# Kernel optimization log

Measured on AMD Instinct MI355X. Metric: run time of the kernel, lower is better.

## Reference

```python
import jax, jax.numpy as jnp
import numpy as np

B, T, C = 4, 2048, 1024
H = 16
D = C // H          # 64 head dim
CS = 128            # chunk_size (hard-coded in module)


def setup_inputs() -> dict:
    key = jax.random.key(0)
    ks = jax.random.split(key, 6)
    scale = 0.02
    x = jax.random.normal(ks[0], (B, T, C), dtype=jnp.float32)
    Wq = jax.random.normal(ks[1], (C, C), dtype=jnp.float32) * scale
    Wk = jax.random.normal(ks[2], (C, C), dtype=jnp.float32) * scale
    Wv = jax.random.normal(ks[3], (C, C), dtype=jnp.float32) * scale
    Wo = jax.random.normal(ks[4], (C, C), dtype=jnp.float32) * scale
    alpha_raw = jnp.zeros((1, H, 1, 1), dtype=jnp.float32)
    beta_raw = jnp.zeros((1, H, 1, 1), dtype=jnp.float32)
    return {"x": x, "Wq": Wq, "Wk": Wk, "Wv": Wv, "Wo": Wo,
            "alpha_raw": alpha_raw, "beta_raw": beta_raw}


def reference(x, Wq, Wk, Wv, Wo, alpha_raw, beta_raw):
    Bb, Tt, Cc = x.shape
    nc = Tt // CS
    N = Bb * H * nc  # flattened (batch, head, chunk) recurrence lanes

    # projections -> [B, H, T, D]
    def proj(W):
        return (x @ W).reshape(Bb, Tt, H, D).transpose(0, 2, 1, 3)
    q, k, v = proj(Wq), proj(Wk), proj(Wv)
    # F.normalize(k, dim=-1) with eps=1e-12
    k = k / jnp.maximum(jnp.linalg.norm(k, axis=-1, keepdims=True), 1e-12)

    alpha = jax.nn.sigmoid(alpha_raw).reshape(H) * 0.5  # [H]
    beta = jax.nn.sigmoid(beta_raw).reshape(H) * 0.5    # [H]
    a = jnp.broadcast_to(alpha[None, :, None], (Bb, H, nc)).reshape(N, 1, 1)
    b = jnp.broadcast_to(beta[None, :, None], (Bb, H, nc)).reshape(N, 1, 1)

    # chunk layout [CS, N, D] for time-major scan
    def to_scan(u):
        return u.reshape(Bb, H, nc, CS, D).reshape(N, CS, D).transpose(1, 0, 2)
    qc, kc, vc = to_scan(q), to_scan(k), to_scan(v)

    # --- per-chunk operators: A = prod(I - a k k^T), B accumulates writes ---
    def op_step(carry, kv):
        A, Bo = carry
        kt, vt = kv  # [N, D]
        Ak = jnp.einsum('nij,nj->ni', A, kt)
        A = A - a * (Ak[:, :, None] * kt[:, None, :])
        Bk = jnp.einsum('nij,nj->ni', Bo, kt)
        Bo = Bo - a * (Bk[:, :, None] * kt[:, None, :]) + b * (vt[:, :, None] * kt[:, None, :])
        return (A, Bo), None

    A0 = jnp.broadcast_to(jnp.eye(D, dtype=x.dtype), (N, D, D))
    (Aop, Bop), _ = jax.lax.scan(op_step, (A0, jnp.zeros((N, D, D), x.dtype)), (kc, vc))

    # --- inter-chunk scan: M_{i+1} = M_i A_i + B_i ---
    Aop_c = Aop.reshape(Bb, H, nc, D, D).transpose(2, 0, 1, 3, 4)
    Bop_c = Bop.reshape(Bb, H, nc, D, D).transpose(2, 0, 1, 3, 4)

    def chunk_step(M, ab):
        Ai, Bi = ab
        return jnp.einsum('bhij,bhjk->bhik', M, Ai) + Bi, M

    M_final, M_starts = jax.lax.scan(
        chunk_step, jnp.zeros((Bb, H, D, D), x.dtype), (Aop_c, Bop_c))

    # --- intra-chunk application: y_t = M_t q_t; rank-1 delta update ---
    M0 = M_starts.transpose(1, 2, 0, 3, 4).reshape(N, D, D)

    def proc_step(M, qkv):
        qt, kt, vt = qkv
        yt = jnp.einsum('nij,nj->ni', M, qt)  # == q_t @ M^T (inference path)
        Mk = jnp.einsum('nij,nj->ni', M, kt)
        M = M - a * (Mk[:, :, None] * kt[:, None, :]) + b * (vt[:, :, None] * kt[:, None, :])
        return M, yt

    _, ys = jax.lax.scan(proc_step, M0, (qc, kc, vc))  # [CS, N, D]
    y = ys.transpose(1, 0, 2).reshape(Bb, H, Tt, D)
    y = y.transpose(0, 2, 1, 3).reshape(Bb, Tt, Cc)
    y = y @ Wo  # c_proj (dropout=0 -> identity)
    return (y, M_final)
```

## Files before the change

### kernel.cpp

```cpp
#include <hip/hip_runtime.h>
#include <stdint.h>


#define DEV __device__ __forceinline__

typedef __attribute__((ext_vector_type(4))) float f32x4;
typedef __attribute__((ext_vector_type(8))) __bf16 bf16x8;
typedef __attribute__((ext_vector_type(4))) __bf16 bf16x4;

typedef const __attribute__((address_space(1))) uint32_t* gas1_t;
typedef __attribute__((address_space(3))) uint32_t* las3_t;

DEV void gload_lds16(const void* g, void* l) {
  __builtin_amdgcn_global_load_lds((gas1_t)g, (las3_t)l, 16, 0, 0);
}

DEV float sgm(float x) { return 1.f / (1.f + __expf(-x)); }

template <int CTRL>
DEV float dpp_mov(float x) {
  return __builtin_bit_cast(
      float, __builtin_amdgcn_mov_dpp(__builtin_bit_cast(int, x), CTRL, 0xF, 0xF, true));
}
DEV float row16_reduce(float x) {
  x += dpp_mov<0x121>(x);
  x += dpp_mov<0x122>(x);
  x += dpp_mov<0x124>(x);
  x += dpp_mov<0x128>(x);
  return x;
}

DEV int swzb(int row, int col, int stride) {
  return ((row * stride + col) << 1) ^ ((row & 7) << 4);
}
DEV bf16x8 ldfrag(const __bf16* B, int row, int col, int stride) {
  return *(const bf16x8*)((const char*)B + swzb(row, col, stride));
}
DEV __bf16 ldsc(const __bf16* B, int row, int col, int stride) {
  return *(const __bf16*)((const char*)B + swzb(row, col, stride));
}
DEV void stb(__bf16* B, int row, int col, int stride, __bf16 v) {
  *(__bf16*)((char*)B + swzb(row, col, stride)) = v;
}
DEV void stb4(__bf16* B, int row, int c4, int stride, bf16x4 v) {
  *(bf16x4*)((char*)B + swzb(row, c4, stride)) = v;
}
DEV int goffn(int tr) {
  int m = tr >> 1;
  return (tr & 1) ? (2 * m * m + 4 * m + 2) : (2 * m * m + 2 * m);
}
DEV int stile(int tr, int sc) { return ((tr * (tr + 1)) / 2 + sc) * 256; }

__global__ __launch_bounds__(256) void cast_f32_bf16(const float* __restrict__ in,
                                                     __bf16* __restrict__ out) {
  int idx = blockIdx.x * 256 + threadIdx.x;
  float4 v = ((const float4*)in)[idx];
  bf16x4 o;
  o[0] = (__bf16)v.x; o[1] = (__bf16)v.y; o[2] = (__bf16)v.z; o[3] = (__bf16)v.w;
  ((bf16x4*)out)[idx] = o;
}

__global__ __launch_bounds__(256) void transpose_cast4(const float* __restrict__ W0,
                                                       const float* __restrict__ W1,
                                                       const float* __restrict__ W2,
                                                       const float* __restrict__ W3,
                                                       __bf16* __restrict__ Wt) {
  const float* W = (blockIdx.z == 0) ? W0 : (blockIdx.z == 1) ? W1
                   : (blockIdx.z == 2) ? W2 : W3;
  __bf16* dst = Wt + ((size_t)blockIdx.z << 20);
  __shared__ float tile[32][33];
  int tx = threadIdx.x & 31, ty = threadIdx.x >> 5;
  int n0 = blockIdx.x * 32, k0 = blockIdx.y * 32;
#pragma unroll
  for (int u = 0; u < 4; ++u)
    tile[ty + u * 8][tx] = W[(size_t)(k0 + ty + u * 8) * 1024 + n0 + tx];
  __syncthreads();
#pragma unroll
  for (int u = 0; u < 4; ++u)
    dst[(size_t)(n0 + ty + u * 8) * 1024 + k0 + tx] = (__bf16)tile[tx][ty + u * 8];
}

DEV int ghash(int row) { return (row ^ (row >> 2)) & 3; }
DEV void stage_tile32(const __bf16* __restrict__ G, __bf16* L, int t, int wid, int K) {
#pragma unroll
  for (int it = 0; it < 2; ++it) {
    int e = it * 256 + t;
    int row = e >> 2;
    int c0 = ((e & 3) ^ ghash(row)) << 3;
    gload_lds16(G + (size_t)row * K + c0, L + it * 2048 + wid * 512);
  }
}
DEV bf16x8 ldfrag32(const __bf16* L, int row, int fkq) {
  return *(const bf16x8*)(L + row * 32 + ((fkq ^ ghash(row)) << 3));
}

__global__ __launch_bounds__(256, 3) void gemm_bt(const __bf16* __restrict__ A,
                                                  const __bf16* __restrict__ Bt,
                                                  float* __restrict__ Cf,
                                                  __bf16* __restrict__ Cb,
                                                  int mode, int NBN) {
  const int t = threadIdx.x;
  const int wid = t >> 6, lane = t & 63;
  const int fr = lane & 15, fkq = lane >> 4;
  const int wr = wid >> 1, wc = wid & 1;
  const int K = 1024;
  int nwg = gridDim.x, lin = blockIdx.x;
  int q = nwg >> 3;
  int id2 = (lin & 7) * q + (lin >> 3);
  int bn = id2 % NBN, bm = id2 / NBN;
  __shared__ __bf16 lA[3][4096];
  __shared__ __bf16 lB[3][4096];
  const __bf16* Ab = A + (size_t)(bm * 128) * K;
  const __bf16* Bb = Bt + (size_t)(bn * 128) * K;
  f32x4 acc[4][4];
#pragma unroll
  for (int m = 0; m < 4; ++m)
#pragma unroll
    for (int nn = 0; nn < 4; ++nn) acc[m][nn] = 0.f;
  stage_tile32(Ab, lA[0], t, wid, K);
  stage_tile32(Bb, lB[0], t, wid, K);
  stage_tile32(Ab + 32, lA[1], t, wid, K);
  stage_tile32(Bb + 32, lB[1], t, wid, K);
  int cur = 0;
  for (int kt = 0; kt < 32; ++kt) {
    asm volatile("s_barrier" ::: "memory");
    if (kt + 2 < 32) {
      int nxt = cur >= 1 ? cur - 1 : cur + 2;
      stage_tile32(Ab + (kt + 2) * 32, lA[nxt], t, wid, K);
      stage_tile32(Bb + (kt + 2) * 32, lB[nxt], t, wid, K);
      asm volatile("s_waitcnt vmcnt(8)" ::: "memory");
    } else if (kt + 1 < 32) {
      asm volatile("s_waitcnt vmcnt(4)" ::: "memory");
    } else {
      asm volatile("s_waitcnt vmcnt(0)" ::: "memory");
    }
    asm volatile("s_barrier" ::: "memory");
    bf16x8 af[4], bg[4];
#pragma unroll
    for (int m = 0; m < 4; ++m)
      af[m] = ldfrag32(lA[cur], wr * 64 + m * 16 + fr, fkq);
#pragma unroll
    for (int nn = 0; nn < 4; ++nn)
      bg[nn] = ldfrag32(lB[cur], wc * 64 + nn * 16 + fr, fkq);
#pragma unroll
    for (int m = 0; m < 4; ++m)
#pragma unroll
      for (int nn = 0; nn < 4; ++nn)
        acc[m][nn] =
            __builtin_amdgcn_mfma_f32_16x16x32_bf16(af[m], bg[nn], acc[m][nn], 0, 0, 0);
    cur = (cur < 2) ? cur + 1 : 0;
  }
#pragma unroll
  for (int m = 0; m < 4; ++m) {
#pragma unroll
    for (int nn = 0; nn < 4; ++nn) {
#pragma unroll
      for (int rg = 0; rg < 4; ++rg) {
        int row = bm * 128 + wr * 64 + m * 16 + fkq * 4 + rg;
        int col = bn * 128 + wc * 64 + nn * 16 + fr;
        float val = acc[m][nn][rg];
        if (mode == 0) {
          Cf[(size_t)row * 1024 + col] = val;
        } else {
          int buf = col >> 10, cc = col & 1023;
          int b = row >> 11, tk = row & 2047;
          int h = cc >> 6, d = cc & 63;
          Cb[(size_t)buf * 8388608 + (((size_t)b * 16 + h) * 2048 + tk) * 64 + d] =
              (__bf16)val;
        }
      }
    }
  }
}

__global__ __launch_bounds__(512, 6) void wy_ab(const __bf16* __restrict__ kb,
                                                const __bf16* __restrict__ vb,
                                                const float* __restrict__ ar,
                                                const float* __restrict__ br,
                                                __bf16* __restrict__ Ug,
                                                __bf16* __restrict__ Wgb,
                                                __bf16* __restrict__ ATg,
                                                __bf16* __restrict__ Bop) {
  int n = blockIdx.x, h = (n >> 4) & 15;
  float a = sgm(ar[h]) * 0.5f;
  float b = sgm(br[h]) * 0.5f;
  int t = threadIdx.x, wid = t >> 6, lane = t & 63;
  int fr = lane & 15, fkq = lane >> 4, fk = fkq * 8;
  __shared__ __attribute__((aligned(16))) char pool[51200];
  __bf16* Ks  = (__bf16*)pool;
  __bf16* MTu = (__bf16*)pool;
  __bf16* MTw = (__bf16*)(pool + 16384);
  __bf16* Sng = (__bf16*)(pool + 32768);
  __bf16* KT  = (__bf16*)(pool + 32768);
  const __bf16* kg = kb + (size_t)n * 8192;
  const __bf16* vg = vb + (size_t)n * 8192;
  bf16x8 zz;
#pragma unroll
  for (int e = 0; e < 8; ++e) zz[e] = (__bf16)0.f;
  f32x4 c0 = {0.f, 0.f, 0.f, 0.f};
  bf16x4 kreg[4];
#pragma unroll
  for (int it = 0; it < 4; ++it) {
    int u = it * 512 + t;
    int row = u >> 4, c4 = (u & 15) * 4;
    bf16x4 kh = ((const bf16x4*)kg)[u];
    float kf[4];
#pragma unroll
    for (int e = 0; e < 4; ++e) kf[e] = (float)kh[e];
    float ssq = kf[0] * kf[0] + kf[1] * kf[1] + kf[2] * kf[2] + kf[3] * kf[3];
    ssq = row16_reduce(ssq);
    float inv = 1.f / fmaxf(sqrtf(ssq), 1e-12f);
    bf16x4 kn;
#pragma unroll
    for (int e = 0; e < 4; ++e) kn[e] = (__bf16)(kf[e] * inv);
    kreg[it] = kn;
    stb4(Ks, row, c4, 64, kn);
  }
  __syncthreads();
  for (int p = wid; p < 36; p += 8) {
    int tr = 0, pp = p;
    while (pp > tr) { pp -= (tr + 1); ++tr; }
    int sc = pp;
    f32x4 acc = {0.f, 0.f, 0.f, 0.f};
#pragma unroll
    for (int ks = 0; ks < 2; ++ks)
      acc = __builtin_amdgcn_mfma_f32_16x16x32_bf16(
          ldfrag(Ks, tr * 16 + fr, ks * 32 + fk, 64),
          ldfrag(Ks, sc * 16 + fr, ks * 32 + fk, 64), acc, 0, 0, 0);
    __bf16* dst = Sng + stile(tr, sc);
#pragma unroll
    for (int rg = 0; rg < 4; ++rg) {
      int r = fkq * 4 + rg;
      float v = -a * acc[rg];
      if (tr == sc && fr >= r) v = 0.f;
      dst[r * 16 + fr] = (__bf16)v;
    }
  }
  f32x4 U[4], W[4];
#pragma unroll
  for (int ct = 0; ct < 4; ++ct) {
#pragma unroll
    for (int rg = 0; rg < 4; ++rg) {
      int row = wid * 16 + fkq * 4 + rg, col = ct * 16 + fr;
      U[ct][rg] = (float)ldsc(Ks, row, col, 64);
      W[ct][rg] = b * (float)vg[row * 64 + col];
    }
  }
  __syncthreads();
  {
    __bf16* scr  = ((__bf16*)pool) + wid * 2048;
    __bf16* tNT  = scr;
    __bf16* tN2R = scr + 256;
    __bf16* tN2T = scr + 512;
    __bf16* tN4R = scr + 768;
    __bf16* tN4T = scr + 1024;
    __bf16* tN8T = scr + 1280;
    __bf16* tPR  = scr + 1536;
    __bf16* Nd = Sng + stile(wid, wid);
    float nv[4];
#pragma unroll
    for (int rg = 0; rg < 4; ++rg) {
      nv[rg] = (float)Nd[(fkq * 4 + rg) * 16 + fr];
      tNT[fr * 16 + fkq * 4 + rg] = (__bf16)nv[rg];
    }
    asm volatile("s_waitcnt lgkmcnt(0)" ::: "memory");
    bf16x8 af = (fk < 16) ? *(const bf16x8*)(Nd + fr * 16 + fk) : zz;
    bf16x8 bop = (fk < 16) ? *(const bf16x8*)(tNT + fr * 16 + fk) : zz;
    f32x4 X = __builtin_amdgcn_mfma_f32_16x16x32_bf16(af, bop, c0, 0, 0, 0);
#pragma unroll
    for (int rg = 0; rg < 4; ++rg) {
      __bf16 v = (__bf16)X[rg];
      tN2R[(fkq * 4 + rg) * 16 + fr] = v;
      tN2T[fr * 16 + fkq * 4 + rg] = v;
    }
    asm volatile("s_waitcnt lgkmcnt(0)" ::: "memory");
    af = (fk < 16) ? *(const bf16x8*)(tN2R + fr * 16 + fk) : zz;
    bop = (fk < 16) ? *(const bf16x8*)(tN2T + fr * 16 + fk) : zz;
    X = __builtin_amdgcn_mfma_f32_16x16x32_bf16(af, bop, c0, 0, 0, 0);
#pragma unroll
    for (int rg = 0; rg < 4; ++rg) {
      __bf16 v = (__bf16)X[rg];
      tN4R[(fkq * 4 + rg) * 16 + fr] = v;
      tN4T[fr * 16 + fkq * 4 + rg] = v;
    }
    asm volatile("s_waitcnt lgkmcnt(0)" ::: "memory");
    af = (fk < 16) ? *(const bf16x8*)(tN4R + fr * 16 + fk) : zz;
    bop = (fk < 16) ? *(const bf16x8*)(tN4T + fr * 16 + fk) : zz;
    X = __builtin_amdgcn_mfma_f32_16x16x32_bf16(af, bop, c0, 0, 0, 0);
#pragma unroll
    for (int rg = 0; rg < 4; ++rg)
      tN8T[fr * 16 + fkq * 4 + rg] = (__bf16)X[rg];
    f32x4 P;
#pragma unroll
    for (int rg = 0; rg < 4; ++rg)
      P[rg] = ((fkq * 4 + rg) == fr ? 1.f : 0.f) + nv[rg];
#pragma unroll
    for (int d = 0; d < 3; ++d) {
      const __bf16* tB = (d == 0) ? tN2T : (d == 1) ? tN4T : tN8T;
#pragma unroll
      for (int rg = 0; rg < 4; ++rg)
        tPR[(fkq * 4 + rg) * 16 + fr] = (__bf16)P[rg];
      asm volatile("s_waitcnt lgkmcnt(0)" ::: "memory");
      af = (fk < 16) ? *(const bf16x8*)(tPR + fr * 16 + fk) : zz;
      bop = (fk < 16) ? *(const bf16x8*)(tB + fr * 16 + fk) : zz;
      P = __builtin_amdgcn_mfma_f32_16x16x32_bf16(af, bop, P, 0, 0, 0);
    }
#pragma unroll
    for (int rg = 0; rg < 4; ++rg)
      Nd[(fkq * 4 + rg) * 16 + fr] = (__bf16)P[rg];
  }
  __syncthreads();
  for (int bb = 0; bb < 8; ++bb) {
    if (wid == bb) {
#pragma unroll
      for (int ct = 0; ct < 4; ++ct) {
        bf16x4 uu, ww;
#pragma unroll
        for (int rg = 0; rg < 4; ++rg) {
          uu[rg] = (__bf16)U[ct][rg];
          ww[rg] = (__bf16)W[ct][rg];
        }
        stb4(MTu, ct * 16 + fr, bb * 16 + fkq * 4, 128, uu);
        stb4(MTw, ct * 16 + fr, bb * 16 + fkq * 4, 128, ww);
      }
      asm volatile("s_waitcnt lgkmcnt(0)" ::: "memory");
      const __bf16* invT = Sng + stile(bb, bb);
      bf16x8 afv = (fk < 16) ? *(const bf16x8*)(invT + fr * 16 + fk) : zz;
#pragma unroll
      for (int ct = 0; ct < 4; ++ct) {
        bf16x8 bu = (fk < 16) ? ldfrag(MTu, ct * 16 + fr, bb * 16 + fk, 128) : zz;
        bf16x8 bw = (fk < 16) ? ldfrag(MTw, ct * 16 + fr, bb * 16 + fk, 128) : zz;
        U[ct] = __builtin_amdgcn_mfma_f32_16x16x32_bf16(afv, bu, c0, 0, 0, 0);
        W[ct] = __builtin_amdgcn_mfma_f32_16x16x32_bf16(afv, bw, c0, 0, 0, 0);
      }
#pragma unroll
      for (int ct = 0; ct < 4; ++ct) {
        bf16x4 uu, ww;
#pragma unroll
        for (int rg = 0; rg < 4; ++rg) {
          uu[rg] = (__bf16)U[ct][rg];
          ww[rg] = (__bf16)W[ct][rg];
        }
        stb4(MTu, ct * 16 + fr, bb * 16 + fkq * 4, 128, uu);
        stb4(MTw, ct * 16 + fr, bb * 16 + fkq * 4, 128, ww);
      }
    }
    __syncthreads();
    if (wid > bb) {
      bf16x8 af = zz;
      if (fk < 16) af = *(const bf16x8*)(Sng + stile(wid, bb) + fr * 16 + fk);
#pragma unroll
      for (int ct = 0; ct < 4; ++ct) {
        bf16x8 bu = zz, bw = zz;
        if (fk < 16) {
          bu = ldfrag(MTu, ct * 16 + fr, bb * 16 + fk, 128);
          bw = ldfrag(MTw, ct * 16 + fr, bb * 16 + fk, 128);
        }
        U[ct] = __builtin_amdgcn_mfma_f32_16x16x32_bf16(af, bu, U[ct], 0, 0, 0);
        W[ct] = __builtin_amdgcn_mfma_f32_16x16x32_bf16(af, bw, W[ct], 0, 0, 0);
      }
    }
  }
#pragma unroll
  for (int it = 0; it < 4; ++it) {
    int u = it * 512 + t;
    int row = u >> 4, c4 = (u & 15) * 4;
#pragma unroll
    for (int e = 0; e < 4; ++e) stb(KT, c4 + e, row, 128, kreg[it][e]);
  }
  __bf16* ugo = Ug + (size_t)n * 8192;
  __bf16* wgo = Wgb + (size_t)n * 8192;
#pragma unroll
  for (int ct = 0; ct < 4; ++ct)
#pragma unroll
    for (int rg = 0; rg < 4; ++rg) {
      int row = wid * 16 + fkq * 4 + rg, col = ct * 16 + fr;
      ugo[row * 64 + col] = (__bf16)U[ct][rg];
      wgo[row * 64 + col] = (__bf16)W[ct][rg];
    }
  __syncthreads();
#pragma unroll
  for (int q = 0; q < 4; ++q) {
    int tile = wid + q * 8;
    int mat = tile >> 4;
    int ti = (tile >> 2) & 3, tj = tile & 3;
    f32x4 acc = {0.f, 0.f, 0.f, 0.f};
    if (mat == 0) {
#pragma unroll
      for (int ks = 0; ks < 4; ++ks)
        acc = __builtin_amdgcn_mfma_f32_16x16x32_bf16(
            ldfrag(KT, ti * 16 + fr, ks * 32 + fk, 128),
            ldfrag(MTu, tj * 16 + fr, ks * 32 + fk, 128), acc, 0, 0, 0);
      char* dst = (char*)(ATg + (size_t)n * 4096);
#pragma unroll
      for (int rg = 0; rg < 4; ++rg) {
        int i = ti * 16 + fkq * 4 + rg, j = tj * 16 + fr;
        float v = (i == j ? 1.f : 0.f) - a * acc[rg];
        *(__bf16*)(dst + swzb(i, j, 64)) = (__bf16)v;
      }
    } else {
#pragma unroll
      for (int ks = 0; ks < 4; ++ks)
        acc = __builtin_amdgcn_mfma_f32_16x16x32_bf16(
            ldfrag(MTw, ti * 16 + fr, ks * 32 + fk, 128),
            ldfrag(KT, tj * 16 + fr, ks * 32 + fk, 128), acc, 0, 0, 0);
      __bf16* dst = Bop + (size_t)n * 4096;
#pragma unroll
      for (int rg = 0; rg < 4; ++rg)
        dst[(ti * 16 + fkq * 4 + rg) * 64 + tj * 16 + fr] = (__bf16)acc[rg];
    }
  }
}

__global__ __launch_bounds__(512) void chunk_scan(const __bf16* __restrict__ ATg,
                                                  const __bf16* __restrict__ Bop,
                                                  __bf16* __restrict__ Mst,
                                                  float* __restrict__ Mfinal) {
  int bh = blockIdx.x;
  int t = threadIdx.x, wid = t >> 6, lane = t & 63;
  int fr = lane & 15, fkq = lane >> 4, fk = fkq * 8;
  int ti = wid & 3, tj0 = (wid >> 2) << 1;
  __shared__ __bf16 Mh[4096];
  __shared__ __bf16 Ml[4096];
  __shared__ __bf16 At[2][4096];
  f32x4 acc[2];
  acc[0] = 0.f;
  acc[1] = 0.f;
  gload_lds16(ATg + (size_t)bh * 16 * 4096 + t * 8, At[0] + t * 8);
  for (int c = 0; c < 16; ++c) {
    int cur = c & 1;
    if (c < 15)
      gload_lds16(ATg + ((size_t)(bh * 16 + c + 1)) * 4096 + t * 8,
                  At[cur ^ 1] + t * 8);
    __bf16* mstc = Mst + ((size_t)(bh * 16 + c)) * 4096;
#pragma unroll
    for (int p = 0; p < 2; ++p) {
      int tj = tj0 + p;
#pragma unroll
      for (int rg = 0; rg < 4; ++rg) {
        int row = ti * 16 + fkq * 4 + rg, col = tj * 16 + fr;
        float v = acc[p][rg];
        __bf16 hi = (__bf16)v;
        mstc[row * 64 + col] = hi;
        stb(Mh, row, col, 64, hi);
        stb(Ml, row, col, 64, (__bf16)(v - (float)hi));
      }
    }
    __syncthreads();
    size_t bb = ((size_t)(bh * 16 + c)) * 4096;
#pragma unroll
    for (int p = 0; p < 2; ++p) {
      int tj = tj0 + p;
      f32x4 na;
#pragma unroll
      for (int rg = 0; rg < 4; ++rg)
        na[rg] = (float)Bop[bb + (ti * 16 + fkq * 4 + rg) * 64 + tj * 16 + fr];
#pragma unroll
      for (int ks = 0; ks < 2; ++ks) {
        bf16x8 bfrag = ldfrag(At[cur], tj * 16 + fr, ks * 32 + fk, 64);
        bf16x8 ah = ldfrag(Mh, ti * 16 + fr, ks * 32 + fk, 64);
        bf16x8 al = ldfrag(Ml, ti * 16 + fr, ks * 32 + fk, 64);
        na = __builtin_amdgcn_mfma_f32_16x16x32_bf16(ah, bfrag, na, 0, 0, 0);
        na = __builtin_amdgcn_mfma_f32_16x16x32_bf16(al, bfrag, na, 0, 0, 0);
      }
      acc[p] = na;
    }
    __syncthreads();
  }
#pragma unroll
  for (int p = 0; p < 2; ++p) {
    int tj = tj0 + p;
#pragma unroll
    for (int rg = 0; rg < 4; ++rg)
      Mfinal[(size_t)bh * 4096 + (ti * 16 + fkq * 4 + rg) * 64 + tj * 16 + fr] =
          acc[p][rg];
  }
}

__global__ __launch_bounds__(512, 4) void y_assemble(const __bf16* __restrict__ qb,
                                                     const __bf16* __restrict__ kb,
                                                     const __bf16* __restrict__ Ug,
                                                     const __bf16* __restrict__ Wgb,
                                                     const __bf16* __restrict__ Mst,
                                                     const float* __restrict__ ar,
                                                     __bf16* __restrict__ ybf) {
  int n = blockIdx.x, h = (n >> 4) & 15, b = n >> 8, c = n & 15;
  float a = sgm(ar[h]) * 0.5f;
  int t = threadIdx.x, wid = t >> 6, lane = t & 63;
  int fr = lane & 15, fk = (lane >> 4) * 8;
  __shared__ __bf16 Qs[8192];
  __shared__ __bf16 Rs[8192];
  __shared__ __bf16 M0s[4096];
  __shared__ __bf16 Gs[10240];
  __shared__ __bf16 WtT[8192];
  const __bf16* qg = qb + (size_t)n * 8192;
  const __bf16* kg = kb + (size_t)n * 8192;
  const __bf16* mg = Mst + (size_t)n * 4096;
#pragma unroll
  for (int it = 0; it < 4; ++it) {
    int u = it * 512 + t;
    int row = u >> 4, c4 = (u & 15) * 4;
    stb4(Qs, row, c4, 64, ((const bf16x4*)qg)[u]);
    bf16x4 kh = ((const bf16x4*)kg)[u];
    float kf[4];
#pragma unroll
    for (int e = 0; e < 4; ++e) kf[e] = (float)kh[e];
    float ssq = kf[0] * kf[0] + kf[1] * kf[1] + kf[2] * kf[2] + kf[3] * kf[3];
    ssq = row16_reduce(ssq);
    float inv = 1.f / fmaxf(sqrtf(ssq), 1e-12f);
    bf16x4 kn;
#pragma unroll
    for (int e = 0; e < 4; ++e) kn[e] = (__bf16)(kf[e] * inv);
    stb4(Rs, row, c4, 64, kn);
  }
#pragma unroll
  for (int it = 0; it < 2; ++it) {
    int u = it * 512 + t;
    int row = u >> 4, c4 = (u & 15) * 4;
    stb4(M0s, row, c4, 64, ((const bf16x4*)mg)[u]);
  }
#pragma unroll
  for (int pz = 0; pz < 2; ++pz) {
    int e = pz * 512 + t;
    int m = e >> 8, idx = e & 255;
    Gs[(2 * m * m + 4 * m + 1) * 256 + idx] = (__bf16)0.f;
  }
  __syncthreads();
  for (int p = wid; p < 36; p += 8) {
    int tr = 0, pp = p;
    while (pp > tr) { pp -= (tr + 1); ++tr; }
    int sc = pp;
    f32x4 acc = {0.f, 0.f, 0.f, 0.f};
#pragma unroll
    for (int ks = 0; ks < 2; ++ks)
      acc = __builtin_amdgcn_mfma_f32_16x16x32_bf16(
          ldfrag(Qs, tr * 16 + fr, ks * 32 + fk, 64),
          ldfrag(Rs, sc * 16 + fr, ks * 32 + fk, 64), acc, 0, 0, 0);
    int row0 = (lane >> 4) * 4, col = lane & 15;
    __bf16* gt = Gs + (goffn(tr) + sc) * 256;
#pragma unroll
    for (int rg = 0; rg < 4; ++rg) {
      int r = row0 + rg;
      float v = acc[rg];
      if (tr == sc && col >= r) v = 0.f;
      gt[r * 16 + col] = (__bf16)v;
    }
  }
  __syncthreads();
  const __bf16* ug = Ug + (size_t)n * 8192;
  const __bf16* wg = Wgb + (size_t)n * 8192;
#pragma unroll
  for (int it = 0; it < 4; ++it) {
    int u = it * 512 + t;
    int row = u >> 4, c4 = (u & 15) * 4;
    stb4(Rs, row, c4, 64, ((const bf16x4*)ug)[u]);
  }
  __syncthreads();
#pragma unroll
  for (int q = 0; q < 4; ++q) {
    int tile = wid + q * 8;
    int ti = tile >> 2, tj = tile & 3;
    f32x4 acc = {0.f, 0.f, 0.f, 0.f};
#pragma unroll
    for (int ks = 0; ks < 2; ++ks)
      acc = __builtin_amdgcn_mfma_f32_16x16x32_bf16(
          ldfrag(Rs, ti * 16 + fr, ks * 32 + fk, 64),
          ldfrag(M0s, tj * 16 + fr, ks * 32 + fk, 64), acc, 0, 0, 0);
    int row0 = (lane >> 4) * 4, col = lane & 15;
#pragma unroll
    for (int rg = 0; rg < 4; ++rg) {
      int s = ti * 16 + row0 + rg, i = tj * 16 + col;
      float wv = (float)wg[s * 64 + i];
      stb(WtT, i, s, 128, (__bf16)(wv - a * acc[rg]));
    }
  }
  __syncthreads();
  __bf16* yg = ybf + ((size_t)(b * 2048 + c * 128)) * 1024 + h * 64;
#pragma unroll
  for (int q = 0; q < 4; ++q) {
    int tile = wid + q * 8;
    int ti = tile >> 2, tj = tile & 3;
    f32x4 acc = {0.f, 0.f, 0.f, 0.f};
#pragma unroll
    for (int ks = 0; ks < 2; ++ks)
      acc = __builtin_amdgcn_mfma_f32_16x16x32_bf16(
          ldfrag(Qs, ti * 16 + fr, ks * 32 + fk, 64),
          ldfrag(M0s, tj * 16 + fr, ks * 32 + fk, 64), acc, 0, 0, 0);
    int goffv = goffn(ti);
    int np = (ti + 2) >> 1;
    for (int ks = 0; ks < np; ++ks) {
      int gtile = goffv + ks * 2 + (fk >> 4);
      bf16x8 af = *(const bf16x8*)(Gs + gtile * 256 + fr * 16 + (fk & 15));
      acc = __builtin_amdgcn_mfma_f32_16x16x32_bf16(
          af, ldfrag(WtT, tj * 16 + fr, ks * 32 + fk, 128), acc, 0, 0, 0);
    }
    int row0 = (lane >> 4) * 4, col = lane & 15;
#pragma unroll
    for (int rg = 0; rg < 4; ++rg) {
      int tt = ti * 16 + row0 + rg, d = tj * 16 + col;
      yg[(size_t)tt * 1024 + d] = (__bf16)acc[rg];
    }
  }
}

extern "C" void kernel_launch(void* const* d_in, const int* in_sizes, int n_in,
                              void* d_out, int out_size, void* d_ws, size_t ws_size,
                              hipStream_t stream) {
  const float* x  = (const float*)d_in[0];
  const float* Wq = (const float*)d_in[1];
  const float* Wk = (const float*)d_in[2];
  const float* Wv = (const float*)d_in[3];
  const float* Wo = (const float*)d_in[4];
  const float* ar = (const float*)d_in[5];
  const float* br = (const float*)d_in[6];

  char* ws = (char*)d_ws;
  __bf16* xb    = (__bf16*)ws;
  __bf16* ybf   = xb;
  __bf16* wqkvt = (__bf16*)(ws + (17u << 20));
  __bf16* wot   = wqkvt + (3u << 20);
  __bf16* qb    = (__bf16*)(ws + (25u << 20));
  __bf16* kb    = qb + 8388608;
  __bf16* vb    = kb + 8388608;
  __bf16* Ugb   = (__bf16*)(ws + (76u << 20));
  __bf16* Wgb   = (__bf16*)(ws + (93u << 20));
  __bf16* ATg   = (__bf16*)(ws + (110u << 20));
  __bf16* Bop   = (__bf16*)(ws + (127u << 20));
  __bf16* Mst   = (__bf16*)(ws + (144u << 20));

  float* yout = (float*)d_out;
  float* Mfin = yout + 8388608;

  cast_f32_bf16<<<8192, 256, 0, stream>>>(x, xb);
  transpose_cast4<<<dim3(32, 32, 4), 256, 0, stream>>>(Wq, Wk, Wv, Wo, wqkvt);

  gemm_bt<<<1536, 256, 0, stream>>>(xb, wqkvt, nullptr, qb, 1, 24);

  wy_ab<<<1024, 512, 0, stream>>>(kb, vb, ar, br, Ugb, Wgb, ATg, Bop);
  chunk_scan<<<64, 512, 0, stream>>>(ATg, Bop, Mst, Mfin);
  y_assemble<<<1024, 512, 0, stream>>>(qb, kb, Ugb, Wgb, Mst, ar, ybf);

  gemm_bt<<<512, 256, 0, stream>>>(ybf, wot, yout, nullptr, 0, 8);
}
```

Measured before the change: 185.2 us.

## Replace QKV projection GEMM with 256x256-tile 8-wave double-buffered kernel

Adds a new QKV projection GEMM that computes a 256x256 output tile per 512-thread workgroup. It stages 64-wide K slices of A and B halves into double-buffered, XOR-swizzled LDS, interleaves the prefetch of the next slice with four MFMA phases, and raises wave priority around the MFMA blocks. The larger tile improves data reuse per LDS byte and cuts the grid from 1536 to 384 blocks, using a grouped block-index remap for L2 locality. The trade-off is heavy register pressure from 32 accumulator fragments per wave and hand-tuned vmcnt waits that must stay correct.

```diff
diff --git a/kernel.cpp b/kernel.cpp
--- a/kernel.cpp
+++ b/kernel.cpp
@@ -78,6 +78,116 @@
 #pragma unroll
   for (int u = 0; u < 4; ++u)
     dst[(size_t)(n0 + ty + u * 8) * 1024 + k0 + tx] = (__bf16)tile[tx][ty + u * 8];
+}
+
+DEV void stage_half(const __bf16* __restrict__ G, __bf16* L, int t, int K) {
+#pragma unroll
+  for (int it = 0; it < 2; ++it) {
+    int e = it * 512 + t;
+    int r = e >> 3;
+    int c0 = ((e & 7) ^ (r & 7)) << 3;
+    gload_lds16(G + (size_t)r * K + c0, L + e * 8);
+  }
+}
+DEV bf16x8 ldh(const __bf16* L, int row, int gq) {
+  return *(const bf16x8*)(L + row * 64 + ((gq ^ (row & 7)) << 3));
+}
+
+#define QKV_PHASE(P, QA, QB, STAGE_STMT, WAIT_STMT)                           \
+  {                                                                           \
+    const __bf16* LAp = lA[cur] + (QA) * 8192;                                \
+    const __bf16* LBp = lB[cur] + (QB) * 8192;                                \
+    bf16x8 af[4][2], bg[2][2];                                                \
+    _Pragma("unroll") for (int m2 = 0; m2 < 4; ++m2)                          \
+        _Pragma("unroll") for (int kk = 0; kk < 2; ++kk)                      \
+            af[m2][kk] = ldh(LAp, wr2 * 64 + m2 * 16 + fr, kk * 4 + fkq);     \
+    _Pragma("unroll") for (int n2 = 0; n2 < 2; ++n2)                          \
+        _Pragma("unroll") for (int kk = 0; kk < 2; ++kk)                      \
+            bg[n2][kk] = ldh(LBp, wc2 * 32 + n2 * 16 + fr, kk * 4 + fkq);     \
+    STAGE_STMT;                                                               \
+    asm volatile("s_barrier" ::: "memory");                                   \
+    WAIT_STMT;                                                                \
+    __builtin_amdgcn_s_setprio(1);                                            \
+    _Pragma("unroll") for (int kk = 0; kk < 2; ++kk)                          \
+        _Pragma("unroll") for (int m2 = 0; m2 < 4; ++m2)                      \
+            _Pragma("unroll") for (int n2 = 0; n2 < 2; ++n2)                  \
+                acc[P][m2][n2] = __builtin_amdgcn_mfma_f32_16x16x32_bf16(     \
+                    af[m2][kk], bg[n2][kk], acc[P][m2][n2], 0, 0, 0);         \
+    __builtin_amdgcn_s_setprio(0);                                            \
+    asm volatile("s_barrier" ::: "memory");                                   \
+  }
+
+__global__ __launch_bounds__(512, 2) void gemm_qkv8(const __bf16* __restrict__ A,
+                                                    const __bf16* __restrict__ Bt,
+                                                    __bf16* __restrict__ Cb) {
+  const int t = threadIdx.x;
+  const int wid = t >> 6, lane = t & 63;
+  const int fr = lane & 15, fkq = lane >> 4;
+  const int wr2 = wid >> 2, wc2 = wid & 3;
+  const int K = 1024;
+  const int NBN = 12;
+  int nwg = gridDim.x, lin = blockIdx.x;
+  int q8 = nwg >> 3;
+  int id2 = (lin & 7) * q8 + (lin >> 3);
+  int bn = id2 % NBN, bm = id2 / NBN;
+  __shared__ __bf16 lA[2][16384];
+  __shared__ __bf16 lB[2][16384];
+  const __bf16* Ab = A + (size_t)(bm * 256) * K;
+  const __bf16* Bb = Bt + (size_t)(bn * 256) * K;
+  f32x4 acc[4][4][2];
+#pragma unroll
+  for (int p = 0; p < 4; ++p)
+#pragma unroll
+    for (int m2 = 0; m2 < 4; ++m2)
+#pragma unroll
+      for (int n2 = 0; n2 < 2; ++n2) acc[p][m2][n2] = 0.f;
+  stage_half(Ab, lA[0], t, K);
+  stage_half(Bb, lB[0], t, K);
+  stage_half(Ab + (size_t)128 * K, lA[0] + 8192, t, K);
+  stage_half(Bb + (size_t)128 * K, lB[0] + 8192, t, K);
+  asm volatile("s_waitcnt vmcnt(4)" ::: "memory");
+  asm volatile("s_barrier" ::: "memory");
+  for (int kt = 0; kt < 15; ++kt) {
+    int cur = kt & 1;
+    const __bf16* An = Ab + (kt + 1) * 64;
+    const __bf16* Bn = Bb + (kt + 1) * 64;
+    __bf16* lAn = lA[cur ^ 1];
+    __bf16* lBn = lB[cur ^ 1];
+    QKV_PHASE(0, 0, 0, stage_half(An, lAn, t, K),
+              asm volatile("s_waitcnt vmcnt(4)" ::: "memory"))
+    QKV_PHASE(1, 1, 0, stage_half(Bn, lBn, t, K),
+              asm volatile("s_waitcnt vmcnt(4)" ::: "memory"))
+    QKV_PHASE(2, 1, 1, stage_half(An + (size_t)128 * K, lAn + 8192, t, K), )
+    QKV_PHASE(3, 0, 1, stage_half(Bn + (size_t)128 * K, lBn + 8192, t, K),
+              asm volatile("s_waitcnt vmcnt(4)" ::: "memory"))
+  }
+  {
+    int cur = 1;
+    QKV_PHASE(0, 0, 0, , asm volatile("s_waitcnt vmcnt(2)" ::: "memory"))
+    QKV_PHASE(1, 1, 0, , asm volatile("s_waitcnt vmcnt(0)" ::: "memory"))
+    QKV_PHASE(2, 1, 1, , )
+    QKV_PHASE(3, 0, 1, , )
+  }
+  const int QAv[4] = {0, 1, 1, 0}, QBv[4] = {0, 0, 1, 1};
+#pragma unroll
+  for (int p = 0; p < 4; ++p) {
+#pragma unroll
+    for (int m2 = 0; m2 < 4; ++m2) {
+#pragma unroll
+      for (int n2 = 0; n2 < 2; ++n2) {
+#pragma unroll
+        for (int rg = 0; rg < 4; ++rg) {
+          int row = bm * 256 + QAv[p] * 128 + wr2 * 64 + m2 * 16 + fkq * 4 + rg;
+          int col = bn * 256 + QBv[p] * 128 + wc2 * 32 + n2 * 16 + fr;
+          int buf = col >> 10, cc = col & 1023;
+          int b = row >> 11, tk = row & 2047;
+          int h = cc >> 6, d = cc & 63;
+          Cb[(size_t)buf * 8388608 + (((size_t)b * 16 + h) * 2048 + tk) * 64 + d] =
+              (__bf16)acc[p][m2][n2][rg];
+        }
+      }
+    }
+  }
 }
 
 DEV int ghash(int row) { return (row ^ (row >> 2)) & 3; }
@@ -634,7 +744,7 @@
   cast_f32_bf16<<<8192, 256, 0, stream>>>(x, xb);
   transpose_cast4<<<dim3(32, 32, 4), 256, 0, stream>>>(Wq, Wk, Wv, Wo, wqkvt);
 
-  gemm_bt<<<1536, 256, 0, stream>>>(xb, wqkvt, nullptr, qb, 1, 24);
+  gemm_qkv8<<<384, 512, 0, stream>>>(xb, wqkvt, qb);
 
   wy_ab<<<1024, 512, 0, stream>>>(kb, vb, ar, br, Ugb, Wgb, ATg, Bop);
   chunk_scan<<<64, 512, 0, stream>>>(ATg, Bop, Mst, Mfin);
```

Measured after the change: 196.7 us. 1.06x slower.
